# Kernel optimization log

Measured on AMD Instinct MI355X. Metric: run time of the kernel, lower is better.

Reference implementation:

```python
import jax, jax.numpy as jnp
import numpy as np

N_NODES = 50000
NFEAT = 512
NHID = 128
N_EDGES = 800000
LN_EPS = 1e-5


def setup_inputs() -> dict:
    key = jax.random.key(0)
    k1, k2, k3, k4, k5 = jax.random.split(key, 5)
    h = jax.random.normal(k1, (N_NODES, NFEAT), dtype=jnp.float32)
    src = jax.random.randint(k2, (N_EDGES,), 0, N_NODES, dtype=jnp.int32)
    dst = jax.random.randint(k3, (N_EDGES,), 0, N_NODES, dtype=jnp.int32)
    # GraphConv params (glorot-ish) + bias; LayerNorm affine params
    W = jax.random.normal(k4, (NFEAT, NHID), dtype=jnp.float32) / np.sqrt(NFEAT)
    b = jnp.zeros((NHID,), dtype=jnp.float32)
    gamma = jnp.ones((NHID,), dtype=jnp.float32)
    beta = jnp.zeros((NHID,), dtype=jnp.float32)
    return {"h": h, "src": src, "dst": dst, "W": W, "b": b, "gamma": gamma, "beta": beta}


def reference(h, src, dst, W, b, gamma, beta):
    n = h.shape[0]
    ones = jnp.ones_like(src, dtype=jnp.float32)
    out_deg = jax.ops.segment_sum(ones, src, num_segments=n)
    in_deg = jax.ops.segment_sum(ones, dst, num_segments=n)
    out_norm = jnp.maximum(out_deg, 1.0) ** -0.5  # [N]
    in_norm = jnp.maximum(in_deg, 1.0) ** -0.5    # [N]

    # norm='both': scale source features by out_deg^{-1/2}
    x = h * out_norm[:, None]
    # in_feats > out_feats -> DGL multiplies by W before aggregation
    x = x @ W  # [N, NHID]
    # sparse aggregate: sum messages over incoming edges
    agg = jax.ops.segment_sum(x[src], dst, num_segments=n)  # [N, NHID]
    agg = agg * in_norm[:, None] + b

    # LayerNorm over last dim
    mu = jnp.mean(agg, axis=-1, keepdims=True)
    var = jnp.mean((agg - mu) ** 2, axis=-1, keepdims=True)
    y = (agg - mu) * jax.lax.rsqrt(var + LN_EPS) * gamma + beta
    return y
```

## Files before the change

### kernel.cpp

```cpp
#include <hip/hip_runtime.h>

#define N_NODES 50000
#define NFEAT   512
#define NHID    128
#define N_EDGES 800000
#define LN_EPS  1e-5f

#define GEMM_ROWS   32
#define GEMM_BLOCKS ((N_NODES + GEMM_ROWS - 1) / GEMM_ROWS)
#define DEG_BLOCKS  (N_EDGES / 256)
#define NB_SCAN     ((N_NODES + 1023) / 1024)

typedef __attribute__((ext_vector_type(8))) short bf16x8;
typedef __attribute__((ext_vector_type(4))) float fx4;

__device__ __forceinline__ unsigned short f2bf(float f) {
    union { float f; unsigned u; } v; v.f = f;
    unsigned r = v.u + 0x7FFF + ((v.u >> 16) & 1);
    return (unsigned short)(r >> 16);
}

__device__ __forceinline__ void bf2x(unsigned u, float& lo, float& hi) {
    union { unsigned u; float f; } a, b;
    a.u = u << 16;
    b.u = u & 0xFFFF0000u;
    lo = a.f; hi = b.f;
}

__global__ __launch_bounds__(256) void prep_kernel(
    const float* __restrict__ W, unsigned short* __restrict__ wf,
    int4* __restrict__ zero_ptr)
{
    int t = blockIdx.x * 256 + threadIdx.x;
#pragma unroll
    for (int i = t; i < 25088; i += 16384)
        zero_ptr[i] = make_int4(0, 0, 0, 0);

    if (blockIdx.x < 32) {
        int lane = t & 63;
        int frag = t >> 6;
        int kc = frag >> 3, tt = frag & 7;
        int n  = tt * 16 + (lane & 15);
        int k0 = kc * 32 + (lane >> 4) * 8;
        unsigned short v[8];
#pragma unroll
        for (int j = 0; j < 8; j++)
            v[j] = f2bf(W[(size_t)(k0 + j) * NHID + n]);
        *(bf16x8*)(wf + (size_t)t * 8) = *(bf16x8*)v;
    }
}

__global__ __launch_bounds__(256) void fused_gemm_degree(
    const float* __restrict__ h, const unsigned short* __restrict__ wf,
    unsigned short* __restrict__ x,
    const int* __restrict__ src, const int* __restrict__ dst,
    int* __restrict__ out_deg, int* __restrict__ in_deg,
    int* __restrict__ edge_pos)
{
    __shared__ __align__(16) unsigned short afrag_lds[2][16 * 64 * 8];

    const int tid = threadIdx.x;
    const int B = blockIdx.x;
    bool isDeg; int id;
    if (B < 2 * GEMM_BLOCKS) { isDeg = (B & 1); id = B >> 1; }
    else                     { isDeg = true;    id = B - GEMM_BLOCKS; }

    if (isDeg) {
        int e = id * 256 + tid;
        int s = src[e];
        int d = dst[e];
        int pos = atomicAdd(&in_deg[d], 1);
        atomicAdd(&out_deg[s], 1);
        edge_pos[e] = pos;
        return;
    }

    const int row0 = id * GEMM_ROWS;

#pragma unroll
    for (int half = 0; half < 2; half++) {
        float4 v[8];
#pragma unroll
        for (int it = 0; it < 8; it++) {
            int i = tid + (half * 8 + it) * 256;
            int r = i >> 7;
            int grow = row0 + r;
            if (grow > N_NODES - 1) grow = N_NODES - 1;
            v[it] = ((const float4*)h)[(size_t)grow * 128 + (i & 127)];
        }
#pragma unroll
        for (int it = 0; it < 8; it++) {
            int i = tid + (half * 8 + it) * 256;
            int r  = i >> 7;
            int g  = r >> 4;
            int rr = r & 15;
            int k0 = (i & 127) << 2;
            int kc = k0 >> 5;
            int q  = (k0 >> 3) & 3;
            int j  = k0 & 7;
            int gp = q * 16 + (rr ^ (q | ((kc & 1) << 2)));
            unsigned long long pk =
                (unsigned long long)f2bf(v[it].x)
              | ((unsigned long long)f2bf(v[it].y) << 16)
              | ((unsigned long long)f2bf(v[it].z) << 32)
              | ((unsigned long long)f2bf(v[it].w) << 48);
            *(unsigned long long*)(&afrag_lds[g][0] + kc * 512 + gp * 8 + j) = pk;
        }
    }
    __syncthreads();

    const int wave = tid >> 6;
    const int lane = tid & 63;
    const int t0   = wave * 2;
    const int rr_l = lane & 15;
    const int q_l  = lane >> 4;
    const int g_e  = q_l * 16 + (rr_l ^ q_l);
    const int g_o  = q_l * 16 + (rr_l ^ q_l ^ 4);

    fx4 acc00 = (fx4){0.f, 0.f, 0.f, 0.f};
    fx4 acc01 = (fx4){0.f, 0.f, 0.f, 0.f};
    fx4 acc10 = (fx4){0.f, 0.f, 0.f, 0.f};
    fx4 acc11 = (fx4){0.f, 0.f, 0.f, 0.f};

    const bf16x8* a0p = (const bf16x8*)&afrag_lds[0][0];
    const bf16x8* a1p = (const bf16x8*)&afrag_lds[1][0];
    const bf16x8* wfp = (const bf16x8*)wf + t0 * 64 + lane;

#pragma unroll 4
    for (int kc = 0; kc < 16; kc++) {
        int gidx = (kc & 1) ? g_o : g_e;
        bf16x8 a0 = a0p[kc * 64 + gidx];
        bf16x8 a1 = a1p[kc * 64 + gidx];
        bf16x8 b0 = wfp[kc * 512];
        bf16x8 b1 = wfp[kc * 512 + 64];
        acc00 = __builtin_amdgcn_mfma_f32_16x16x32_bf16(a0, b0, acc00, 0, 0, 0);
        acc01 = __builtin_amdgcn_mfma_f32_16x16x32_bf16(a0, b1, acc01, 0, 0, 0);
        acc10 = __builtin_amdgcn_mfma_f32_16x16x32_bf16(a1, b0, acc10, 0, 0, 0);
        acc11 = __builtin_amdgcn_mfma_f32_16x16x32_bf16(a1, b1, acc11, 0, 0, 0);
    }

    __syncthreads();
    unsigned short* orow = (unsigned short*)&afrag_lds[0][0];
    {
        const int q = lane >> 4;
        const int c = lane & 15;
#pragma unroll
        for (int reg = 0; reg < 4; reg++) {
            int r0 = q * 4 + reg;
            orow[r0 * 128 + t0 * 16 + c]              = f2bf(acc00[reg]);
            orow[r0 * 128 + (t0 + 1) * 16 + c]        = f2bf(acc01[reg]);
            orow[(16 + r0) * 128 + t0 * 16 + c]       = f2bf(acc10[reg]);
            orow[(16 + r0) * 128 + (t0 + 1) * 16 + c] = f2bf(acc11[reg]);
        }
    }
    __syncthreads();
    {
        const int4* osrc = (const int4*)&afrag_lds[0][0];
#pragma unroll
        for (int p = 0; p < 2; p++) {
            int idx = tid + p * 256;
            int r   = idx >> 4;
            int gr  = row0 + r;
            if (gr < N_NODES)
                ((int4*)x)[(size_t)gr * 16 + (idx & 15)] = osrc[idx];
        }
    }
}

__global__ __launch_bounds__(1024) void scan_local(
    const int* __restrict__ in_deg, int* __restrict__ row_ptr, int* __restrict__ bsum,
    const int* __restrict__ out_deg, float* __restrict__ out_norm)
{
    __shared__ int wsum[16];
    const int tid = threadIdx.x;
    const int lane = tid & 63, wave = tid >> 6;
    int i = blockIdx.x * 1024 + tid;
    int v = (i < N_NODES) ? in_deg[i] : 0;
    int sv = v;
#pragma unroll
    for (int off = 1; off < 64; off <<= 1) {
        int t = __shfl_up(sv, off);
        if (lane >= off) sv += t;
    }
    if (lane == 63) wsum[wave] = sv;
    if (i < N_NODES)
        out_norm[i] = rsqrtf(fmaxf((float)out_deg[i], 1.0f));
    __syncthreads();
    if (wave == 0) {
        int wv = (lane < 16) ? wsum[lane] : 0;
#pragma unroll
        for (int off = 1; off < 16; off <<= 1) {
            int t = __shfl_up(wv, off);
            if (lane >= off) wv += t;
        }
        if (lane < 16) wsum[lane] = wv;
    }
    __syncthreads();
    int excl = ((wave > 0) ? wsum[wave - 1] : 0) + (sv - v);
    if (i < N_NODES) row_ptr[i] = excl;
    if (tid == 1023) bsum[blockIdx.x] = wsum[15];
}

__global__ __launch_bounds__(1024) void scan_add2(
    int* __restrict__ row_ptr, const int* __restrict__ bsum)
{
    __shared__ int off_s, tot_s;
    const int tid = threadIdx.x;
    if (tid < 64) {
        int v = (tid < NB_SCAN) ? bsum[tid] : 0;
        int sv = v;
#pragma unroll
        for (int off = 1; off < 64; off <<= 1) {
            int t = __shfl_up(sv, off);
            if (tid >= off) sv += t;
        }
        int pre = __shfl(sv, (blockIdx.x == 0) ? 0 : (blockIdx.x - 1));
        int tot = __shfl(sv, NB_SCAN - 1);
        if (tid == 0) {
            off_s = (blockIdx.x == 0) ? 0 : pre;
            tot_s = tot;
        }
    }
    __syncthreads();
    int i = blockIdx.x * 1024 + tid;
    if (i < N_NODES) row_ptr[i] += off_s;
    if (blockIdx.x == 0 && tid == 0) row_ptr[N_NODES] = tot_s;
}

__global__ __launch_bounds__(256) void fill_kernel(
    const int* __restrict__ src, const int* __restrict__ dst,
    const int* __restrict__ row_ptr, const int* __restrict__ edge_pos,
    int* __restrict__ csr_src)
{
    int e = blockIdx.x * 256 + threadIdx.x;
    if (e < N_EDGES) {
        int d = dst[e];
        csr_src[row_ptr[d] + edge_pos[e]] = src[e];
    }
}

#define ACC4(uu, ww) {                                                    \
    float p0,p1,p2,p3,p4,p5,p6,p7;                                        \
    bf2x(uu.x,p0,p1); bf2x(uu.y,p2,p3);                                   \
    bf2x(uu.z,p4,p5); bf2x(uu.w,p6,p7);                                   \
    a0 += p0*ww; a1 += p1*ww; a2 += p2*ww; a3 += p3*ww;                   \
    a4 += p4*ww; a5 += p5*ww; a6 += p6*ww; a7 += p7*ww; }

__global__ __launch_bounds__(256) void aggregate_kernel(
    const unsigned short* __restrict__ x, const int* __restrict__ row_ptr,
    const int* __restrict__ csr_src, const float* __restrict__ out_norm,
    const float* __restrict__ b, const float* __restrict__ gamma,
    const float* __restrict__ beta, float* __restrict__ out)
{
    const int n    = blockIdx.x * 4 + (threadIdx.x >> 6);
    const int lane = threadIdx.x & 63;
    const int qi   = lane >> 4;
    const int c    = lane & 15;
    const int start = row_ptr[n];
    const int end   = row_ptr[n + 1];

    float a0 = 0.f, a1 = 0.f, a2 = 0.f, a3 = 0.f;
    float a4 = 0.f, a5 = 0.f, a6 = 0.f, a7 = 0.f;

    for (int base = start; base < end; base += 64) {
        int  me   = base + lane;
        bool vld  = (me < end);
        int  msrc = vld ? csr_src[me] : 0;
        float mw  = vld ? out_norm[msrc] : 0.f;
        int cnt = min(64, end - base);
        int ng  = (cnt + 3) >> 2;
        int g = 0;
        for (; g + 4 <= ng; g += 4) {
            int i0 = 4 * g + qi, i1 = i0 + 4, i2 = i0 + 8, i3 = i0 + 12;
            int s0 = __shfl(msrc, i0);
            int s1 = __shfl(msrc, i1);
            int s2 = __shfl(msrc, i2);
            int s3 = __shfl(msrc, i3);
            float w0 = __shfl(mw, i0);
            float w1 = __shfl(mw, i1);
            float w2 = __shfl(mw, i2);
            float w3 = __shfl(mw, i3);
            uint4 u0 = *(const uint4*)(x + (size_t)s0 * NHID + c * 8);
            uint4 u1 = *(const uint4*)(x + (size_t)s1 * NHID + c * 8);
            uint4 u2 = *(const uint4*)(x + (size_t)s2 * NHID + c * 8);
            uint4 u3 = *(const uint4*)(x + (size_t)s3 * NHID + c * 8);
            ACC4(u0, w0) ACC4(u1, w1) ACC4(u2, w2) ACC4(u3, w3)
        }
        for (; g < ng; ++g) {
            int i0 = 4 * g + qi;
            int s0 = __shfl(msrc, i0);
            float w0 = __shfl(mw, i0);
            uint4 u0 = *(const uint4*)(x + (size_t)s0 * NHID + c * 8);
            ACC4(u0, w0)
        }
    }

    a0 += __shfl_xor(a0, 16); a0 += __shfl_xor(a0, 32);
    a1 += __shfl_xor(a1, 16); a1 += __shfl_xor(a1, 32);
    a2 += __shfl_xor(a2, 16); a2 += __shfl_xor(a2, 32);
    a3 += __shfl_xor(a3, 16); a3 += __shfl_xor(a3, 32);
    a4 += __shfl_xor(a4, 16); a4 += __shfl_xor(a4, 32);
    a5 += __shfl_xor(a5, 16); a5 += __shfl_xor(a5, 32);
    a6 += __shfl_xor(a6, 16); a6 += __shfl_xor(a6, 32);
    a7 += __shfl_xor(a7, 16); a7 += __shfl_xor(a7, 32);

    float inorm = rsqrtf(fmaxf((float)(end - start), 1.0f));
    float4 b0 = *(const float4*)(b + c * 8);
    float4 b1 = *(const float4*)(b + c * 8 + 4);
    float v0 = a0 * inorm + b0.x;
    float v1 = a1 * inorm + b0.y;
    float v2 = a2 * inorm + b0.z;
    float v3 = a3 * inorm + b0.w;
    float v4 = a4 * inorm + b1.x;
    float v5 = a5 * inorm + b1.y;
    float v6 = a6 * inorm + b1.z;
    float v7 = a7 * inorm + b1.w;

    float s = ((v0 + v1) + (v2 + v3)) + ((v4 + v5) + (v6 + v7));
#pragma unroll
    for (int off = 8; off > 0; off >>= 1) s += __shfl_xor(s, off);
    float mu = s * (1.0f / 128.0f);

    float d0 = v0 - mu, d1 = v1 - mu, d2 = v2 - mu, d3 = v3 - mu;
    float d4 = v4 - mu, d5 = v5 - mu, d6 = v6 - mu, d7 = v7 - mu;
    float qd = ((d0*d0 + d1*d1) + (d2*d2 + d3*d3)) + ((d4*d4 + d5*d5) + (d6*d6 + d7*d7));
#pragma unroll
    for (int off = 8; off > 0; off >>= 1) qd += __shfl_xor(qd, off);
    float var = qd * (1.0f / 128.0f);
    float rs = rsqrtf(var + LN_EPS);

    if (lane < 16) {
        float4 gg = *(const float4*)(gamma + c * 8);
        float4 be = *(const float4*)(beta + c * 8);
        float4 o;
        o.x = d0 * rs * gg.x + be.x;
        o.y = d1 * rs * gg.y + be.y;
        o.z = d2 * rs * gg.z + be.z;
        o.w = d3 * rs * gg.w + be.w;
        *(float4*)(out + (size_t)n * NHID + c * 8) = o;
    } else if (lane < 32) {
        float4 gg = *(const float4*)(gamma + c * 8 + 4);
        float4 be = *(const float4*)(beta + c * 8 + 4);
        float4 o;
        o.x = d4 * rs * gg.x + be.x;
        o.y = d5 * rs * gg.y + be.y;
        o.z = d6 * rs * gg.z + be.z;
        o.w = d7 * rs * gg.w + be.w;
        *(float4*)(out + (size_t)n * NHID + c * 8 + 4) = o;
    }
}

extern "C" void kernel_launch(void* const* d_in, const int* in_sizes, int n_in,
                              void* d_out, int out_size, void* d_ws, size_t ws_size,
                              hipStream_t stream) {
    const float* h     = (const float*)d_in[0];
    const int*   src   = (const int*)d_in[1];
    const int*   dst   = (const int*)d_in[2];
    const float* W     = (const float*)d_in[3];
    const float* b     = (const float*)d_in[4];
    const float* gamma = (const float*)d_in[5];
    const float* beta  = (const float*)d_in[6];
    float* out = (float*)d_out;

    char* ws = (char*)d_ws;
    const size_t DEG_BYTES = 200704;
    const size_t RP_BYTES  = 200960;
    int*            out_deg  = (int*)(ws);
    int*            in_deg   = (int*)(ws + DEG_BYTES);
    int*            row_ptr  = (int*)(ws + 2 * DEG_BYTES);
    float*          out_norm = (float*)(ws + 2 * DEG_BYTES + RP_BYTES);
    int*            bsum     = (int*)(ws + 3 * DEG_BYTES + RP_BYTES);
    int*            edge_pos = (int*)(ws + 3 * DEG_BYTES + RP_BYTES + 1024);
    int*            csr_src  = (int*)(ws + 3 * DEG_BYTES + RP_BYTES + 1024 + (size_t)N_EDGES * 4);
    unsigned short* wf       = (unsigned short*)(ws + 3 * DEG_BYTES + RP_BYTES + 1024 + 2 * (size_t)N_EDGES * 4);
    unsigned short* x        = (unsigned short*)(ws + 3 * DEG_BYTES + RP_BYTES + 1024 + 2 * (size_t)N_EDGES * 4 + 131072);

    prep_kernel<<<64, 256, 0, stream>>>(W, wf, (int4*)ws);
    fused_gemm_degree<<<GEMM_BLOCKS + DEG_BLOCKS, 256, 0, stream>>>(
        h, wf, x, src, dst, out_deg, in_deg, edge_pos);
    scan_local<<<NB_SCAN, 1024, 0, stream>>>(in_deg, row_ptr, bsum, out_deg, out_norm);
    scan_add2 <<<NB_SCAN, 1024, 0, stream>>>(row_ptr, bsum);
    fill_kernel<<<(N_EDGES + 255) / 256, 256, 0, stream>>>(src, dst, row_ptr, edge_pos, csr_src);
    aggregate_kernel<<<N_NODES / 4, 256, 0, stream>>>(
        x, row_ptr, csr_src, out_norm, b, gamma, beta, out);
}
```

Before: 253.7 us.

## Privatize degree histograms per XCD with workgroup-scope atomics

Replaces the single global in/out-degree counters with eight per-XCD copies, selected from the hardware XCC id register. The counters are updated with relaxed workgroup-scope atomics, so increments can stay in each XCD's own L2 instead of needing device-wide coherence. The scan then merges the copies and stores per-XCD prefix offsets, and the CSR fill uses those offsets to place each edge. In exchange it zeroes and reads eight times more counter memory, writes an extra offset array, and does one more random read per edge in the fill. It also relies on workgroup-scope atomics between different blocks on the same XCD staying coherent.

```diff
diff --git a/kernel.cpp b/kernel.cpp
--- a/kernel.cpp
+++ b/kernel.cpp
@@ -11,6 +11,11 @@
 #define DEG_BLOCKS  (N_EDGES / 256)
 #define NB_SCAN     ((N_NODES + 1023) / 1024)
 
+#define DEG_STRIDE  50176
+#define NXCD        8
+
+#define HWREG_XCC_ID 6164
+
 typedef __attribute__((ext_vector_type(8))) short bf16x8;
 typedef __attribute__((ext_vector_type(4))) float fx4;
 
@@ -33,7 +38,7 @@
 {
     int t = blockIdx.x * 256 + threadIdx.x;
 #pragma unroll
-    for (int i = t; i < 25088; i += 16384)
+    for (int i = t; i < 200704; i += 16384)
         zero_ptr[i] = make_int4(0, 0, 0, 0);
 
     if (blockIdx.x < 32) {
@@ -54,7 +59,7 @@
     const float* __restrict__ h, const unsigned short* __restrict__ wf,
     unsigned short* __restrict__ x,
     const int* __restrict__ src, const int* __restrict__ dst,
-    int* __restrict__ out_deg, int* __restrict__ in_deg,
+    int* __restrict__ out_deg_x, int* __restrict__ in_deg_x,
     int* __restrict__ edge_pos)
 {
     __shared__ __align__(16) unsigned short afrag_lds[2][16 * 64 * 8];
@@ -66,12 +71,17 @@
     else                     { isDeg = true;    id = B - GEMM_BLOCKS; }
 
     if (isDeg) {
+        int xcd = __builtin_amdgcn_s_getreg(HWREG_XCC_ID) & 7;
+        int* my_in  = in_deg_x  + xcd * DEG_STRIDE;
+        int* my_out = out_deg_x + xcd * DEG_STRIDE;
         int e = id * 256 + tid;
         int s = src[e];
         int d = dst[e];
-        int pos = atomicAdd(&in_deg[d], 1);
-        atomicAdd(&out_deg[s], 1);
-        edge_pos[e] = pos;
+        int pos = __hip_atomic_fetch_add(&my_in[d], 1,
+                      __ATOMIC_RELAXED, __HIP_MEMORY_SCOPE_WORKGROUP);
+        __hip_atomic_fetch_add(&my_out[s], 1,
+                      __ATOMIC_RELAXED, __HIP_MEMORY_SCOPE_WORKGROUP);
+        edge_pos[e] = (xcd << 24) | pos;
         return;
     }
 
@@ -168,14 +178,29 @@
 }
 
 __global__ __launch_bounds__(1024) void scan_local(
-    const int* __restrict__ in_deg, int* __restrict__ row_ptr, int* __restrict__ bsum,
-    const int* __restrict__ out_deg, float* __restrict__ out_norm)
+    const int* __restrict__ in_deg_x, int* __restrict__ row_ptr, int* __restrict__ bsum,
+    const int* __restrict__ out_deg_x, float* __restrict__ out_norm,
+    int* __restrict__ xoff)
 {
     __shared__ int wsum[16];
     const int tid = threadIdx.x;
     const int lane = tid & 63, wave = tid >> 6;
     int i = blockIdx.x * 1024 + tid;
-    int v = (i < N_NODES) ? in_deg[i] : 0;
+    int v = 0;
+    if (i < N_NODES) {
+        int acc = 0;
+#pragma unroll
+        for (int xx = 0; xx < NXCD; xx++) {
+            xoff[xx * DEG_STRIDE + i] = acc;
+            acc += in_deg_x[xx * DEG_STRIDE + i];
+        }
+        v = acc;
+        int od = 0;
+#pragma unroll
+        for (int xx = 0; xx < NXCD; xx++)
+            od += out_deg_x[xx * DEG_STRIDE + i];
+        out_norm[i] = rsqrtf(fmaxf((float)od, 1.0f));
+    }
     int sv = v;
 #pragma unroll
     for (int off = 1; off < 64; off <<= 1) {
@@ -183,8 +208,6 @@
         if (lane >= off) sv += t;
     }
     if (lane == 63) wsum[wave] = sv;
-    if (i < N_NODES)
-        out_norm[i] = rsqrtf(fmaxf((float)out_deg[i], 1.0f));
     __syncthreads();
     if (wave == 0) {
         int wv = (lane < 16) ? wsum[lane] : 0;
@@ -230,12 +253,15 @@
 __global__ __launch_bounds__(256) void fill_kernel(
     const int* __restrict__ src, const int* __restrict__ dst,
     const int* __restrict__ row_ptr, const int* __restrict__ edge_pos,
-    int* __restrict__ csr_src)
+    const int* __restrict__ xoff, int* __restrict__ csr_src)
 {
     int e = blockIdx.x * 256 + threadIdx.x;
     if (e < N_EDGES) {
         int d = dst[e];
-        csr_src[row_ptr[d] + edge_pos[e]] = src[e];
+        unsigned ep = (unsigned)edge_pos[e];
+        int xcd = ep >> 24;
+        int pos = ep & 0xFFFFFF;
+        csr_src[row_ptr[d] + xoff[xcd * DEG_STRIDE + d] + pos] = src[e];
     }
 }
 
@@ -362,25 +388,25 @@
     const float* beta  = (const float*)d_in[6];
     float* out = (float*)d_out;
 
-    char* ws = (char*)d_ws;
-    const size_t DEG_BYTES = 200704;
-    const size_t RP_BYTES  = 200960;
-    int*            out_deg  = (int*)(ws);
-    int*            in_deg   = (int*)(ws + DEG_BYTES);
-    int*            row_ptr  = (int*)(ws + 2 * DEG_BYTES);
-    float*          out_norm = (float*)(ws + 2 * DEG_BYTES + RP_BYTES);
-    int*            bsum     = (int*)(ws + 3 * DEG_BYTES + RP_BYTES);
-    int*            edge_pos = (int*)(ws + 3 * DEG_BYTES + RP_BYTES + 1024);
-    int*            csr_src  = (int*)(ws + 3 * DEG_BYTES + RP_BYTES + 1024 + (size_t)N_EDGES * 4);
-    unsigned short* wf       = (unsigned short*)(ws + 3 * DEG_BYTES + RP_BYTES + 1024 + 2 * (size_t)N_EDGES * 4);
-    unsigned short* x        = (unsigned short*)(ws + 3 * DEG_BYTES + RP_BYTES + 1024 + 2 * (size_t)N_EDGES * 4 + 131072);
-
-    prep_kernel<<<64, 256, 0, stream>>>(W, wf, (int4*)ws);
+    char* p = (char*)d_ws;
+    const size_t DEG8_BYTES = (size_t)NXCD * DEG_STRIDE * 4;
+    int*            out_deg_x = (int*)p;            p += DEG8_BYTES;
+    int*            in_deg_x  = (int*)p;            p += DEG8_BYTES;
+    int*            xoff      = (int*)p;            p += DEG8_BYTES;
+    int*            row_ptr   = (int*)p;            p += 200960;
+    float*          out_norm  = (float*)p;          p += 200704;
+    int*            bsum      = (int*)p;            p += 1024;
+    int*            edge_pos  = (int*)p;            p += (size_t)N_EDGES * 4;
+    int*            csr_src   = (int*)p;            p += (size_t)N_EDGES * 4;
+    unsigned short* wf        = (unsigned short*)p; p += 131072;
+    unsigned short* x         = (unsigned short*)p;
+
+    prep_kernel<<<64, 256, 0, stream>>>(W, wf, (int4*)d_ws);
     fused_gemm_degree<<<GEMM_BLOCKS + DEG_BLOCKS, 256, 0, stream>>>(
-        h, wf, x, src, dst, out_deg, in_deg, edge_pos);
-    scan_local<<<NB_SCAN, 1024, 0, stream>>>(in_deg, row_ptr, bsum, out_deg, out_norm);
+        h, wf, x, src, dst, out_deg_x, in_deg_x, edge_pos);
+    scan_local<<<NB_SCAN, 1024, 0, stream>>>(in_deg_x, row_ptr, bsum, out_deg_x, out_norm, xoff);
     scan_add2 <<<NB_SCAN, 1024, 0, stream>>>(row_ptr, bsum);
-    fill_kernel<<<(N_EDGES + 255) / 256, 256, 0, stream>>>(src, dst, row_ptr, edge_pos, csr_src);
+    fill_kernel<<<(N_EDGES + 255) / 256, 256, 0, stream>>>(src, dst, row_ptr, edge_pos, xoff, csr_src);
     aggregate_kernel<<<N_NODES / 4, 256, 0, stream>>>(
         x, row_ptr, csr_src, out_norm, b, gamma, beta, out);
 }
```

New measurement: 257.6 us. About the same (+1.5%).

## Fold out-degree norm into GEMM epilogue and split degree counting from GEMM

Applied to the files above, without the earlier changes.

Degree counting is split out of the fused GEMM+degree kernel into its own kernel, which handles four edges per thread. The GEMM now runs after the scan so it can scale each output row by out_norm before the bf16 store. The aggregation then becomes a plain sum, with no per-edge out_norm gather or weight shuffles, and padding lanes point at a zeroed extra row instead of using a validity mask. The cost is that the GEMM can no longer overlap with the degree atomics, and the node-feature loads move onto the serialized critical path.

```diff
diff --git a/kernel.cpp b/kernel.cpp
--- a/kernel.cpp
+++ b/kernel.cpp
@@ -8,8 +8,8 @@
 
 #define GEMM_ROWS   32
 #define GEMM_BLOCKS ((N_NODES + GEMM_ROWS - 1) / GEMM_ROWS)
-#define DEG_BLOCKS  (N_EDGES / 256)
 #define NB_SCAN     ((N_NODES + 1023) / 1024)
+#define ZROW        N_NODES
 
 typedef __attribute__((ext_vector_type(8))) short bf16x8;
 typedef __attribute__((ext_vector_type(4))) float fx4;
@@ -29,12 +29,15 @@
 
 __global__ __launch_bounds__(256) void prep_kernel(
     const float* __restrict__ W, unsigned short* __restrict__ wf,
-    int4* __restrict__ zero_ptr)
+    int4* __restrict__ zero_ptr, unsigned short* __restrict__ x)
 {
     int t = blockIdx.x * 256 + threadIdx.x;
 #pragma unroll
     for (int i = t; i < 25088; i += 16384)
         zero_ptr[i] = make_int4(0, 0, 0, 0);
+
+    if (blockIdx.x == 63 && threadIdx.x < 16)
+        ((int4*)(x + (size_t)ZROW * NHID))[threadIdx.x] = make_int4(0, 0, 0, 0);
 
     if (blockIdx.x < 32) {
         int lane = t & 63;
@@ -50,47 +53,127 @@
     }
 }
 
-__global__ __launch_bounds__(256) void fused_gemm_degree(
-    const float* __restrict__ h, const unsigned short* __restrict__ wf,
-    unsigned short* __restrict__ x,
+__global__ __launch_bounds__(256) void degree_kernel(
     const int* __restrict__ src, const int* __restrict__ dst,
     int* __restrict__ out_deg, int* __restrict__ in_deg,
     int* __restrict__ edge_pos)
 {
+    int t = blockIdx.x * 256 + threadIdx.x;
+    if (t >= N_EDGES / 4) return;
+    int4 s4 = ((const int4*)src)[t];
+    int4 d4 = ((const int4*)dst)[t];
+    int p0 = atomicAdd(&in_deg[d4.x], 1);
+    int p1 = atomicAdd(&in_deg[d4.y], 1);
+    int p2 = atomicAdd(&in_deg[d4.z], 1);
+    int p3 = atomicAdd(&in_deg[d4.w], 1);
+    atomicAdd(&out_deg[s4.x], 1);
+    atomicAdd(&out_deg[s4.y], 1);
+    atomicAdd(&out_deg[s4.z], 1);
+    atomicAdd(&out_deg[s4.w], 1);
+    ((int4*)edge_pos)[t] = make_int4(p0, p1, p2, p3);
+}
+
+__global__ __launch_bounds__(1024) void scan_local(
+    const int* __restrict__ in_deg, int* __restrict__ row_ptr, int* __restrict__ bsum,
+    const int* __restrict__ out_deg, float* __restrict__ out_norm)
+{
+    __shared__ int wsum[16];
+    const int tid = threadIdx.x;
+    const int lane = tid & 63, wave = tid >> 6;
+    int i = blockIdx.x * 1024 + tid;
+    int v = (i < N_NODES) ? in_deg[i] : 0;
+    int sv = v;
+#pragma unroll
+    for (int off = 1; off < 64; off <<= 1) {
+        int t = __shfl_up(sv, off);
+        if (lane >= off) sv += t;
+    }
+    if (lane == 63) wsum[wave] = sv;
+    if (i < N_NODES)
+        out_norm[i] = rsqrtf(fmaxf((float)out_deg[i], 1.0f));
+    __syncthreads();
+    if (wave == 0) {
+        int wv = (lane < 16) ? wsum[lane] : 0;
+#pragma unroll
+        for (int off = 1; off < 16; off <<= 1) {
+            int t = __shfl_up(wv, off);
+            if (lane >= off) wv += t;
+        }
+        if (lane < 16) wsum[lane] = wv;
+    }
+    __syncthreads();
+    int excl = ((wave > 0) ? wsum[wave - 1] : 0) + (sv - v);
+    if (i < N_NODES) row_ptr[i] = excl;
+    if (tid == 1023) bsum[blockIdx.x] = wsum[15];
+}
+
+__global__ __launch_bounds__(1024) void scan_add2(
+    int* __restrict__ row_ptr, const int* __restrict__ bsum)
+{
+    __shared__ int off_s, tot_s;
+    const int tid = threadIdx.x;
+    if (tid < 64) {
+        int v = (tid < NB_SCAN) ? bsum[tid] : 0;
+        int sv = v;
+#pragma unroll
+        for (int off = 1; off < 64; off <<= 1) {
+            int t = __shfl_up(sv, off);
+            if (tid >= off) sv += t;
+        }
+        int pre = __shfl(sv, (blockIdx.x == 0) ? 0 : (blockIdx.x - 1));
+        int tot = __shfl(sv, NB_SCAN - 1);
+        if (tid == 0) {
+            off_s = (blockIdx.x == 0) ? 0 : pre;
+            tot_s = tot;
+        }
+    }
+    __syncthreads();
+    int i = blockIdx.x * 1024 + tid;
+    if (i < N_NODES) row_ptr[i] += off_s;
+    if (blockIdx.x == 0 && tid == 0) row_ptr[N_NODES] = tot_s;
+}
+
+__global__ __launch_bounds__(256) void fill_kernel(
+    const int* __restrict__ src, const int* __restrict__ dst,
+    const int* __restrict__ row_ptr, const int* __restrict__ edge_pos,
+    int* __restrict__ csr_src)
+{
+    int e = blockIdx.x * 256 + threadIdx.x;
+    if (e < N_EDGES) {
+        int d = dst[e];
+        csr_src[row_ptr[d] + edge_pos[e]] = src[e];
+    }
+}
+
+__global__ __launch_bounds__(256) void gemm_kernel(
+    const float* __restrict__ h, const unsigned short* __restrict__ wf,
+    const float* __restrict__ out_norm, unsigned short* __restrict__ x)
+{
     __shared__ __align__(16) unsigned short afrag_lds[2][16 * 64 * 8];
-
-    const int tid = threadIdx.x;
-    const int B = blockIdx.x;
-    bool isDeg; int id;
-    if (B < 2 * GEMM_BLOCKS) { isDeg = (B & 1); id = B >> 1; }
-    else                     { isDeg = true;    id = B - GEMM_BLOCKS; }
-
-    if (isDeg) {
-        int e = id * 256 + tid;
-        int s = src[e];
-        int d = dst[e];
-        int pos = atomicAdd(&in_deg[d], 1);
-        atomicAdd(&out_deg[s], 1);
-        edge_pos[e] = pos;
-        return;
-    }
-
-    const int row0 = id * GEMM_ROWS;
-
-#pragma unroll
-    for (int half = 0; half < 2; half++) {
-        float4 v[8];
-#pragma unroll
-        for (int it = 0; it < 8; it++) {
-            int i = tid + (half * 8 + it) * 256;
+    __shared__ float on_s[32];
+
+    const int tid  = threadIdx.x;
+    const int row0 = blockIdx.x * GEMM_ROWS;
+
+    if (tid < 32) {
+        int gr = row0 + tid;
+        if (gr > N_NODES - 1) gr = N_NODES - 1;
+        on_s[tid] = out_norm[gr];
+    }
+
+    {
+        float4 v[16];
+#pragma unroll
+        for (int it = 0; it < 16; it++) {
+            int i = tid + it * 256;
             int r = i >> 7;
             int grow = row0 + r;
             if (grow > N_NODES - 1) grow = N_NODES - 1;
             v[it] = ((const float4*)h)[(size_t)grow * 128 + (i & 127)];
         }
 #pragma unroll
-        for (int it = 0; it < 8; it++) {
-            int i = tid + (half * 8 + it) * 256;
+        for (int it = 0; it < 16; it++) {
+            int i = tid + it * 256;
             int r  = i >> 7;
             int g  = r >> 4;
             int rr = r & 15;
@@ -147,10 +230,12 @@
 #pragma unroll
         for (int reg = 0; reg < 4; reg++) {
             int r0 = q * 4 + reg;
-            orow[r0 * 128 + t0 * 16 + c]              = f2bf(acc00[reg]);
-            orow[r0 * 128 + (t0 + 1) * 16 + c]        = f2bf(acc01[reg]);
-            orow[(16 + r0) * 128 + t0 * 16 + c]       = f2bf(acc10[reg]);
-            orow[(16 + r0) * 128 + (t0 + 1) * 16 + c] = f2bf(acc11[reg]);
+            float w0 = on_s[r0];
+            float w1 = on_s[16 + r0];
+            orow[r0 * 128 + t0 * 16 + c]              = f2bf(acc00[reg] * w0);
+            orow[r0 * 128 + (t0 + 1) * 16 + c]        = f2bf(acc01[reg] * w0);
+            orow[(16 + r0) * 128 + t0 * 16 + c]       = f2bf(acc10[reg] * w1);
+            orow[(16 + r0) * 128 + (t0 + 1) * 16 + c] = f2bf(acc11[reg] * w1);
         }
     }
     __syncthreads();
@@ -167,88 +252,16 @@
     }
 }
 
-__global__ __launch_bounds__(1024) void scan_local(
-    const int* __restrict__ in_deg, int* __restrict__ row_ptr, int* __restrict__ bsum,
-    const int* __restrict__ out_deg, float* __restrict__ out_norm)
-{
-    __shared__ int wsum[16];
-    const int tid = threadIdx.x;
-    const int lane = tid & 63, wave = tid >> 6;
-    int i = blockIdx.x * 1024 + tid;
-    int v = (i < N_NODES) ? in_deg[i] : 0;
-    int sv = v;
-#pragma unroll
-    for (int off = 1; off < 64; off <<= 1) {
-        int t = __shfl_up(sv, off);
-        if (lane >= off) sv += t;
-    }
-    if (lane == 63) wsum[wave] = sv;
-    if (i < N_NODES)
-        out_norm[i] = rsqrtf(fmaxf((float)out_deg[i], 1.0f));
-    __syncthreads();
-    if (wave == 0) {
-        int wv = (lane < 16) ? wsum[lane] : 0;
-#pragma unroll
-        for (int off = 1; off < 16; off <<= 1) {
-            int t = __shfl_up(wv, off);
-            if (lane >= off) wv += t;
-        }
-        if (lane < 16) wsum[lane] = wv;
-    }
-    __syncthreads();
-    int excl = ((wave > 0) ? wsum[wave - 1] : 0) + (sv - v);
-    if (i < N_NODES) row_ptr[i] = excl;
-    if (tid == 1023) bsum[blockIdx.x] = wsum[15];
-}
-
-__global__ __launch_bounds__(1024) void scan_add2(
-    int* __restrict__ row_ptr, const int* __restrict__ bsum)
-{
-    __shared__ int off_s, tot_s;
-    const int tid = threadIdx.x;
-    if (tid < 64) {
-        int v = (tid < NB_SCAN) ? bsum[tid] : 0;
-        int sv = v;
-#pragma unroll
-        for (int off = 1; off < 64; off <<= 1) {
-            int t = __shfl_up(sv, off);
-            if (tid >= off) sv += t;
-        }
-        int pre = __shfl(sv, (blockIdx.x == 0) ? 0 : (blockIdx.x - 1));
-        int tot = __shfl(sv, NB_SCAN - 1);
-        if (tid == 0) {
-            off_s = (blockIdx.x == 0) ? 0 : pre;
-            tot_s = tot;
-        }
-    }
-    __syncthreads();
-    int i = blockIdx.x * 1024 + tid;
-    if (i < N_NODES) row_ptr[i] += off_s;
-    if (blockIdx.x == 0 && tid == 0) row_ptr[N_NODES] = tot_s;
-}
-
-__global__ __launch_bounds__(256) void fill_kernel(
-    const int* __restrict__ src, const int* __restrict__ dst,
-    const int* __restrict__ row_ptr, const int* __restrict__ edge_pos,
-    int* __restrict__ csr_src)
-{
-    int e = blockIdx.x * 256 + threadIdx.x;
-    if (e < N_EDGES) {
-        int d = dst[e];
-        csr_src[row_ptr[d] + edge_pos[e]] = src[e];
-    }
-}
-
-#define ACC4(uu, ww) {                                                    \
+#define ACC4(uu) {                                                        \
     float p0,p1,p2,p3,p4,p5,p6,p7;                                        \
     bf2x(uu.x,p0,p1); bf2x(uu.y,p2,p3);                                   \
     bf2x(uu.z,p4,p5); bf2x(uu.w,p6,p7);                                   \
-    a0 += p0*ww; a1 += p1*ww; a2 += p2*ww; a3 += p3*ww;                   \
-    a4 += p4*ww; a5 += p5*ww; a6 += p6*ww; a7 += p7*ww; }
+    a0 += p0; a1 += p1; a2 += p2; a3 += p3;                               \
+    a4 += p4; a5 += p5; a6 += p6; a7 += p7; }
 
 __global__ __launch_bounds__(256) void aggregate_kernel(
     const unsigned short* __restrict__ x, const int* __restrict__ row_ptr,
-    const int* __restrict__ csr_src, const float* __restrict__ out_norm,
+    const int* __restrict__ csr_src,
     const float* __restrict__ b, const float* __restrict__ gamma,
     const float* __restrict__ beta, float* __restrict__ out)
 {
@@ -264,9 +277,7 @@
 
     for (int base = start; base < end; base += 64) {
         int  me   = base + lane;
-        bool vld  = (me < end);
-        int  msrc = vld ? csr_src[me] : 0;
-        float mw  = vld ? out_norm[msrc] : 0.f;
+        int  msrc = (me < end) ? csr_src[me] : (int)ZROW;
         int cnt = min(64, end - base);
         int ng  = (cnt + 3) >> 2;
         int g = 0;
@@ -276,22 +287,17 @@
             int s1 = __shfl(msrc, i1);
             int s2 = __shfl(msrc, i2);
             int s3 = __shfl(msrc, i3);
-            float w0 = __shfl(mw, i0);
-            float w1 = __shfl(mw, i1);
-            float w2 = __shfl(mw, i2);
-            float w3 = __shfl(mw, i3);
             uint4 u0 = *(const uint4*)(x + (size_t)s0 * NHID + c * 8);
             uint4 u1 = *(const uint4*)(x + (size_t)s1 * NHID + c * 8);
             uint4 u2 = *(const uint4*)(x + (size_t)s2 * NHID + c * 8);
             uint4 u3 = *(const uint4*)(x + (size_t)s3 * NHID + c * 8);
-            ACC4(u0, w0) ACC4(u1, w1) ACC4(u2, w2) ACC4(u3, w3)
+            ACC4(u0) ACC4(u1) ACC4(u2) ACC4(u3)
         }
         for (; g < ng; ++g) {
             int i0 = 4 * g + qi;
             int s0 = __shfl(msrc, i0);
-            float w0 = __shfl(mw, i0);
             uint4 u0 = *(const uint4*)(x + (size_t)s0 * NHID + c * 8);
-            ACC4(u0, w0)
+            ACC4(u0)
         }
     }
 
@@ -375,12 +381,13 @@
     unsigned short* wf       = (unsigned short*)(ws + 3 * DEG_BYTES + RP_BYTES + 1024 + 2 * (size_t)N_EDGES * 4);
     unsigned short* x        = (unsigned short*)(ws + 3 * DEG_BYTES + RP_BYTES + 1024 + 2 * (size_t)N_EDGES * 4 + 131072);
 
-    prep_kernel<<<64, 256, 0, stream>>>(W, wf, (int4*)ws);
-    fused_gemm_degree<<<GEMM_BLOCKS + DEG_BLOCKS, 256, 0, stream>>>(
-        h, wf, x, src, dst, out_deg, in_deg, edge_pos);
+    prep_kernel<<<64, 256, 0, stream>>>(W, wf, (int4*)ws, x);
+    degree_kernel<<<(N_EDGES / 4 + 255) / 256, 256, 0, stream>>>(
+        src, dst, out_deg, in_deg, edge_pos);
     scan_local<<<NB_SCAN, 1024, 0, stream>>>(in_deg, row_ptr, bsum, out_deg, out_norm);
     scan_add2 <<<NB_SCAN, 1024, 0, stream>>>(row_ptr, bsum);
     fill_kernel<<<(N_EDGES + 255) / 256, 256, 0, stream>>>(src, dst, row_ptr, edge_pos, csr_src);
+    gemm_kernel<<<GEMM_BLOCKS, 256, 0, stream>>>(h, wf, out_norm, x);
     aggregate_kernel<<<N_NODES / 4, 256, 0, stream>>>(
-        x, row_ptr, csr_src, out_norm, b, gamma, beta, out);
-}
+        x, row_ptr, csr_src, b, gamma, beta, out);
+}
```

Measured after the change: 296.9 us. 1.17x slower.
